# Optimization experiments

Measured on AMD Instinct MI355X. Metric: run time of the kernel, lower is better.

The kernel has to match this reference:

```python
import jax, jax.numpy as jnp
import numpy as np

D = 1024
B = 16
T = 2048
LN_EPS = 1e-5


def setup_inputs() -> dict:
    key = jax.random.key(0)
    k_x, k_in, k_st = jax.random.split(key, 3)
    x = jax.random.normal(k_x, (B, T, D), dtype=jnp.float32)
    # nn.Linear(d, 2d, bias=False): weight [2D, D], y = x @ W.T
    s_in = 1.0 / np.sqrt(D)
    W_in = jax.random.uniform(k_in, (2 * D, D), dtype=jnp.float32, minval=-s_in, maxval=s_in)
    W_state = jax.random.uniform(k_st, (D, D), dtype=jnp.float32, minval=-s_in, maxval=s_in)
    gamma = jnp.ones((D,), dtype=jnp.float32)
    beta = jnp.zeros((D,), dtype=jnp.float32)
    return {"x": x, "W_in": W_in, "W_state": W_state, "gamma": gamma, "beta": beta}


def _glru(x, W_in, W_state, gamma, beta):
    # Batched projections over all timesteps (gates depend only on x).
    proj = jnp.einsum("btd,ed->bte", x, W_in)            # [B, T, 2D]
    gx, vx = jnp.split(proj, 2, axis=-1)                   # each [B, T, D]
    u = jax.nn.sigmoid(gx)                                  # [B, T, D]
    cand = jnp.einsum("btd,ed->bte", vx, W_state)        # [B, T, D]

    # Sequential diagonal linear recurrence: h_t = u_t * h_{t-1} + (1-u_t)*cand_t
    def step(h, uc):
        u_t, c_t = uc
        h = u_t * h + (1.0 - u_t) * c_t
        return h, h

    h0 = jnp.zeros((x.shape[0], x.shape[2]), dtype=x.dtype)
    us = jnp.swapaxes(u, 0, 1)       # [T, B, D]
    cs = jnp.swapaxes(cand, 0, 1)    # [T, B, D]
    _, ys = jax.lax.scan(step, h0, (us, cs))
    y = jnp.swapaxes(ys, 0, 1)       # [B, T, D]

    # LayerNorm over last dim
    mu = jnp.mean(y, axis=-1, keepdims=True)
    var = jnp.mean(jnp.square(y - mu), axis=-1, keepdims=True)
    return (y - mu) * jax.lax.rsqrt(var + LN_EPS) * gamma + beta


def reference(x, W_in, W_state, gamma, beta):
    return _glru(x, W_in, W_state, gamma, beta)
```

## Files before the change

### kernel.cpp

```cpp
#include <hip/hip_runtime.h>

#define D_DIM 1024
#define B_DIM 16
#define T_DIM 2048
#define M_TOT (B_DIM * T_DIM)
#define K_DIM 1024
#define LN_EPS 1e-5f
#define CHUNK 16
#define NCH (T_DIM / CHUNK)

typedef _Float16 half8 __attribute__((ext_vector_type(8)));
typedef _Float16 half4v __attribute__((ext_vector_type(4)));
typedef float f32x4 __attribute__((ext_vector_type(4)));


__global__ __launch_bounds__(256) void prep_all(const float* __restrict__ x,
                                                const float* __restrict__ W_in,
                                                const float* __restrict__ W_state,
                                                _Float16* __restrict__ xh,
                                                _Float16* __restrict__ pk,
                                                _Float16* __restrict__ wvxT,
                                                _Float16* __restrict__ wst) {
    __shared__ _Float16 t[32][33];
    int b = blockIdx.x, tid = threadIdx.x;
    if (b < 2048) {
        int i = b * 256 + tid;
        for (; i < M_TOT * K_DIM / 8; i += 2048 * 256) {
            const float4* p = (const float4*)x + 2 * (size_t)i;
            float4 a = p[0], c = p[1];
            half8 h;
            h[0] = (_Float16)a.x; h[1] = (_Float16)a.y; h[2] = (_Float16)a.z; h[3] = (_Float16)a.w;
            h[4] = (_Float16)c.x; h[5] = (_Float16)c.y; h[6] = (_Float16)c.z; h[7] = (_Float16)c.w;
            ((half8*)xh)[i] = h;
        }
    } else if (b < 2560) {
        int i = (b - 2048) * 256 + tid;
        int ll = i & 63, u = i >> 6;
        int kt = u & 31, nf = u >> 5;
        int n = nf * 16 + (ll & 15);
        int k = kt * 32 + (ll >> 4) * 8;
        const float4* s = (const float4*)&W_in[(size_t)n * 1024 + k];
        float4 a = s[0], c = s[1];
        half8 h;
        h[0] = (_Float16)a.x; h[1] = (_Float16)a.y; h[2] = (_Float16)a.z; h[3] = (_Float16)a.w;
        h[4] = (_Float16)c.x; h[5] = (_Float16)c.y; h[6] = (_Float16)c.z; h[7] = (_Float16)c.w;
        *(half8*)&pk[(size_t)i * 8] = h;
    } else if (b < 3072) {
        int i = (b - 2560) * 256 + tid;
        const float4* p = (const float4*)W_state + 2 * (size_t)i;
        float4 a = p[0], c = p[1];
        half8 h;
        h[0] = (_Float16)a.x; h[1] = (_Float16)a.y; h[2] = (_Float16)a.z; h[3] = (_Float16)a.w;
        h[4] = (_Float16)c.x; h[5] = (_Float16)c.y; h[6] = (_Float16)c.z; h[7] = (_Float16)c.w;
        ((half8*)wst)[i] = h;
    } else {
        int tile = b - 3072;
        int bx = (tile & 31) * 32, by = (tile >> 5) * 32;
        int tx = tid & 31, ty = tid >> 5;
        const float* src = W_in + (size_t)D_DIM * K_DIM;
#pragma unroll
        for (int j = 0; j < 4; ++j)
            t[ty + 8 * j][tx] = (_Float16)src[(size_t)(by + ty + 8 * j) * 1024 + bx + tx];
        __syncthreads();
#pragma unroll
        for (int j = 0; j < 4; ++j)
            wvxT[(size_t)(bx + ty + 8 * j) * 1024 + by + tx] = t[tx][ty + 8 * j];
    }
}

__device__ __forceinline__ void gl_lds16(const _Float16* g, _Float16* l) {
    __builtin_amdgcn_global_load_lds(
        (const __attribute__((address_space(1))) unsigned int*)g,
        (__attribute__((address_space(3))) unsigned int*)l,
        16, 0, 0);
}

__device__ __forceinline__ void stageA32(const _Float16* __restrict__ G,
                                         int row0, int kt,
                                         _Float16* lds0, int wid, int lane) {
    int c = wid * 64 + lane;
    int rl = c >> 2;
    int cc = c & 3;
    int src = cc ^ ((rl >> 1) & 3);
    gl_lds16(G + (size_t)(row0 + rl) * 1024 + kt + src * 8,
             lds0 + (size_t)(wid * 64) * 8);
}

__device__ __forceinline__ half8 frag32(const _Float16* base, int row, int kq) {
    int cc = kq ^ ((row >> 1) & 3);
    return *(const half8*)(base + (size_t)row * 32 + cc * 8);
}

__device__ __forceinline__ half8 bload(const _Float16* __restrict__ pb,
                                       int nf, int kt, int lane) {
    return *(const half8*)(pb + (((size_t)nf * 32 + kt) * 64 + lane) * 8);
}

template <int TA>
__device__ __forceinline__ void gstep(const _Float16* __restrict__ A,
                                      const _Float16* __restrict__ pb,
                                      int m0, int nf0, int t, int nkt,
                                      int wid, int lane, int r, int kq,
                                      _Float16 (&As)[3][64][32],
                                      half8 (&bb)[4],
                                      f32x4 (&acc)[4][4]) {
    half8 ra[4];

    if (t + 1 < nkt) asm volatile("s_waitcnt vmcnt(5)" ::: "memory");
    else             asm volatile("s_waitcnt vmcnt(0)" ::: "memory");
    __builtin_amdgcn_s_barrier();
    __builtin_amdgcn_sched_barrier(0);

#pragma unroll
    for (int mi = 0; mi < 4; mi++) ra[mi] = frag32(&As[TA][0][0], mi * 16 + r, kq);
    if (t + 2 < nkt) stageA32(A, m0, (t + 2) << 5, &As[(TA + 2) % 3][0][0], wid, lane);
    __builtin_amdgcn_s_setprio(1);
#pragma unroll
    for (int mi = 0; mi < 4; mi++)
#pragma unroll
        for (int ni = 0; ni < 4; ni++)
            acc[mi][ni] = __builtin_amdgcn_mfma_f32_16x16x32_f16(ra[mi], bb[ni], acc[mi][ni], 0, 0, 0);
    __builtin_amdgcn_s_setprio(0);
    if (t + 1 < nkt) {
        bb[0] = bload(pb, nf0,      t + 1, lane);
        bb[1] = bload(pb, nf0 + 1,  t + 1, lane);
        bb[2] = bload(pb, nf0 + 64, t + 1, lane);
        bb[3] = bload(pb, nf0 + 65, t + 1, lane);
    }
    __builtin_amdgcn_s_barrier();
}

__global__ __launch_bounds__(256, 3) void gemm256(const _Float16* __restrict__ A,
                                                  const _Float16* __restrict__ pk,
                                                  _Float16* __restrict__ out_u,
                                                  _Float16* __restrict__ out_c,
                                                  float* __restrict__ Ac,
                                                  float* __restrict__ Bc) {
    __shared__ _Float16 As[3][64][32];

    int bid = blockIdx.x;
    int xcd = bid & 7, lin = bid >> 3;
    int mt = xcd * 64 + (lin >> 3);
    int nt = lin & 7;
    int m0 = mt * 64;

    int tid = threadIdx.x, wid = tid >> 6, lane = tid & 63;
    int wc = wid;
    int r = lane & 15, kq = lane >> 4;
    int nf0 = nt * 8 + wc * 2;

    f32x4 acc[4][4];
#pragma unroll
    for (int i = 0; i < 4; i++)
#pragma unroll
        for (int j = 0; j < 4; j++) acc[i][j] = (f32x4)0.f;

    half8 bb[4];
    const int nkt = K_DIM >> 5;

    stageA32(A, m0, 0,  &As[0][0][0], wid, lane);
    stageA32(A, m0, 32, &As[1][0][0], wid, lane);
    bb[0] = bload(pk, nf0,      0, lane);
    bb[1] = bload(pk, nf0 + 1,  0, lane);
    bb[2] = bload(pk, nf0 + 64, 0, lane);
    bb[3] = bload(pk, nf0 + 65, 0, lane);

    for (int t0 = 0; t0 < nkt; t0 += 3) {
        gstep<0>(A, pk, m0, nf0, t0, nkt, wid, lane, r, kq, As, bb, acc);
        if (t0 + 1 < nkt)
            gstep<1>(A, pk, m0, nf0, t0 + 1, nkt, wid, lane, r, kq, As, bb, acc);
        if (t0 + 2 < nkt)
            gstep<2>(A, pk, m0, nf0, t0 + 2, nkt, wid, lane, r, kq, As, bb, acc);
    }

    int rr = kq * 4;
#pragma unroll
    for (int mi = 0; mi < 4; mi++) {
        int mbase = m0 + mi * 16 + rr;
        float Aab[2] = {1.f, 1.f}, Bab[2] = {0.f, 0.f};
#pragma unroll
        for (int ni = 0; ni < 2; ni++) {
            int d = nt * 128 + wc * 32 + ni * 16 + r;
#pragma unroll
            for (int q = 0; q < 4; q++) {
                float u = 1.f / (1.f + __expf(-acc[mi][ni][q]));
                float c = acc[mi][ni + 2][q];
                size_t m = (size_t)(mbase + q);
                out_u[m * D_DIM + d] = (_Float16)u;
                out_c[m * D_DIM + d] = (_Float16)c;
                Bab[ni] = fmaf(u, Bab[ni], (1.f - u) * c);
                Aab[ni] *= u;
            }
        }
#pragma unroll
        for (int ni = 0; ni < 2; ni++) {
            float Aa = Aab[ni], Bb = Bab[ni];
            float oA = __shfl_xor(Aa, 16), oB = __shfl_xor(Bb, 16);
            if (kq & 1) { Bb = fmaf(Aa, oB, Bb); Aa *= oA; }
            else        { Bb = fmaf(oA, Bb, oB); Aa *= oA; }
            oA = __shfl_xor(Aa, 32); oB = __shfl_xor(Bb, 32);
            if (kq & 2) { Bb = fmaf(Aa, oB, Bb); Aa *= oA; }
            else        { Bb = fmaf(oA, Bb, oB); Aa *= oA; }
            if (kq == 0) {
                int d = nt * 128 + wc * 32 + ni * 16 + r;
                int bc = mt * 4 + mi;
                Ac[(size_t)bc * 1024 + d] = Aa;
                Bc[(size_t)bc * 1024 + d] = Bb;
            }
        }
    }
}

__global__ __launch_bounds__(256) void wcomb_splitk(const _Float16* __restrict__ A,
                                                    const _Float16* __restrict__ Bm,
                                                    float* __restrict__ part) {
    __shared__ _Float16 As[128 * 32];
    __shared__ _Float16 Bs[128 * 32];
    int bid = blockIdx.x;
    int mt = bid & 7, nt = (bid >> 3) & 7, sl = bid >> 6;
    int m0 = mt * 128, n0 = nt * 128, kbeg = sl * 256;
    int tid = threadIdx.x, wid = tid >> 6, lane = tid & 63;
    int wr = wid >> 1, wc = wid & 1;

    f32x4 acc[4][4];
#pragma unroll
    for (int i = 0; i < 4; i++)
#pragma unroll
        for (int j = 0; j < 4; j++) acc[i][j] = (f32x4)0.f;

    int r = lane & 15, kq = lane >> 4;

    for (int kt = kbeg; kt < kbeg + 256; kt += 32) {
        __syncthreads();
#pragma unroll
        for (int j = 0; j < 2; ++j) {
            int f = j * 256 + tid;
            int row = f >> 2, kc = f & 3;
            gl_lds16(A + (size_t)(m0 + row) * 1024 + kt + kc * 8, As + (size_t)(j * 256 + wid * 64) * 8);
            gl_lds16(Bm + (size_t)(n0 + row) * 1024 + kt + kc * 8, Bs + (size_t)(j * 256 + wid * 64) * 8);
        }
        __syncthreads();
        half8 af[4], bf[4];
#pragma unroll
        for (int mi = 0; mi < 4; mi++) af[mi] = *(const half8*)&As[(wr * 64 + mi * 16 + r) * 32 + kq * 8];
#pragma unroll
        for (int ni = 0; ni < 4; ni++) bf[ni] = *(const half8*)&Bs[(wc * 64 + ni * 16 + r) * 32 + kq * 8];
#pragma unroll
        for (int mi = 0; mi < 4; mi++)
#pragma unroll
            for (int ni = 0; ni < 4; ni++)
                acc[mi][ni] = __builtin_amdgcn_mfma_f32_16x16x32_f16(af[mi], bf[ni], acc[mi][ni], 0, 0, 0);
    }

    int rr = kq * 4;
    float* pbp = part + (size_t)sl * 1048576;
#pragma unroll
    for (int mi = 0; mi < 4; mi++) {
        int mbase = m0 + wr * 64 + mi * 16 + rr;
#pragma unroll
        for (int ni = 0; ni < 4; ni++) {
            int n = n0 + wc * 64 + ni * 16 + r;
#pragma unroll
            for (int q = 0; q < 4; q++)
                pbp[(size_t)(mbase + q) * 1024 + n] = acc[mi][ni][q];
        }
    }
}

__global__ __launch_bounds__(256) void wcomb_combine_pack(const float* __restrict__ part,
                                                          _Float16* __restrict__ pk) {
    int i = blockIdx.x * 256 + threadIdx.x;
    int ll = i & 63, u = i >> 6;
    int kt = u & 31, nf = u >> 5;
    int e = nf * 16 + (ll & 15);
    int k = kt * 32 + (ll >> 4) * 8;
    size_t o = (size_t)e * 1024 + k;
    float s[8];
#pragma unroll
    for (int j = 0; j < 8; ++j) s[j] = 0.f;
#pragma unroll
    for (int sl = 0; sl < 4; ++sl) {
        const float4* p = (const float4*)&part[(size_t)sl * 1048576 + o];
        float4 a = p[0], c = p[1];
        s[0] += a.x; s[1] += a.y; s[2] += a.z; s[3] += a.w;
        s[4] += c.x; s[5] += c.y; s[6] += c.z; s[7] += c.w;
    }
    half8 h;
#pragma unroll
    for (int j = 0; j < 8; ++j) h[j] = (_Float16)s[j];
    *(half8*)&pk[1048576 + (size_t)i * 8] = h;
}

__global__ __launch_bounds__(256) void scan_pass2(const float* __restrict__ Ac,
                                                  const float* __restrict__ Bc,
                                                  float* __restrict__ h0w) {
    int idx = blockIdx.x * 256 + threadIdx.x;
    int b = idx >> 10, d = idx & (D_DIM - 1);
    float h = 0.f;
#pragma unroll 8
    for (int ch = 0; ch < NCH; ++ch) {
        size_t k = ((size_t)(b * NCH + ch) << 10) + d;
        float a = Ac[k];
        float bv = Bc[k];
        h0w[k] = h;
        h = fmaf(a, h, bv);
    }
}

__global__ __launch_bounds__(64) void scan_ln(const _Float16* __restrict__ u,
                                              const _Float16* __restrict__ cd,
                                              const float* __restrict__ h0,
                                              const float* __restrict__ gamma,
                                              const float* __restrict__ beta,
                                              float* __restrict__ outp) {
    int bc = blockIdx.x;
    int b = bc >> 7, ch = bc & (NCH - 1);
    int lane = threadIdx.x;
    int d0 = lane * 16;
    size_t base = ((size_t)b * T_DIM + (size_t)ch * CHUNK) * D_DIM + d0;

    float g[16], be[16], h[16];
#pragma unroll
    for (int j = 0; j < 16; j += 4) {
        *(float4*)&g[j]  = *(const float4*)&gamma[d0 + j];
        *(float4*)&be[j] = *(const float4*)&beta[d0 + j];
    }
    size_t o = (size_t)bc * D_DIM + d0;
#pragma unroll
    for (int j = 0; j < 16; j += 4) *(float4*)&h[j] = *(const float4*)&h0[o + j];

    half8 ua = *(const half8*)&u[base];
    half8 ub = *(const half8*)&u[base + 8];
    half8 ca = *(const half8*)&cd[base];
    half8 cb = *(const half8*)&cd[base + 8];

#pragma unroll
    for (int t = 0; t < CHUNK; ++t) {
        half8 nua, nub, nca, ncb;
        if (t + 1 < CHUNK) {
            size_t nrow = base + (size_t)(t + 1) * D_DIM;
            nua = *(const half8*)&u[nrow];
            nub = *(const half8*)&u[nrow + 8];
            nca = *(const half8*)&cd[nrow];
            ncb = *(const half8*)&cd[nrow + 8];
        }
        size_t row = base + (size_t)t * D_DIM;
        float s = 0.f, q = 0.f;
#pragma unroll
        for (int j = 0; j < 8; ++j) {
            float ut = (float)ua[j], ct = (float)ca[j];
            h[j] = fmaf(ut, h[j] - ct, ct);
            s += h[j]; q += h[j] * h[j];
        }
#pragma unroll
        for (int j = 0; j < 8; ++j) {
            float ut = (float)ub[j], ct = (float)cb[j];
            h[8 + j] = fmaf(ut, h[8 + j] - ct, ct);
            s += h[8 + j]; q += h[8 + j] * h[8 + j];
        }
#pragma unroll
        for (int off = 32; off > 0; off >>= 1) {
            s += __shfl_xor(s, off);
            q += __shfl_xor(q, off);
        }
        float mu = s * (1.f / D_DIM);
        float var = q * (1.f / D_DIM) - mu * mu;
        float rs = rsqrtf(var + LN_EPS);
        float o16[16];
#pragma unroll
        for (int j = 0; j < 16; ++j) o16[j] = (h[j] - mu) * rs * g[j] + be[j];
#pragma unroll
        for (int j = 0; j < 16; j += 4) *(float4*)&outp[row + j] = *(float4*)&o16[j];
        ua = nua; ub = nub; ca = nca; cb = ncb;
    }
}

extern "C" void kernel_launch(void* const* d_in, const int* in_sizes, int n_in,
                              void* d_out, int out_size, void* d_ws, size_t ws_size,
                              hipStream_t stream) {
    const float* x       = (const float*)d_in[0];
    const float* W_in    = (const float*)d_in[1];
    const float* W_state = (const float*)d_in[2];
    const float* gamma   = (const float*)d_in[3];
    const float* beta    = (const float*)d_in[4];
    float* out = (float*)d_out;

    char* w = (char*)d_ws;
    size_t off = 0;
    auto carve = [&](size_t bytes) {
        void* p = w + off;
        off += (bytes + 255) & ~(size_t)255;
        return p;
    };
    _Float16* xh   = (_Float16*)carve((size_t)M_TOT * K_DIM * 2);
    _Float16* pk   = (_Float16*)carve((size_t)2 * D_DIM * K_DIM * 2);
    _Float16* uarr = (_Float16*)carve((size_t)M_TOT * D_DIM * 2);
    _Float16* cand = (_Float16*)carve((size_t)M_TOT * D_DIM * 2);
    char* scratch  = (char*)carve((size_t)16 * 1024 * 1024);
    _Float16* wvxT = (_Float16*)scratch;
    _Float16* wst  = (_Float16*)(scratch + 2 * 1024 * 1024);
    float* Ac = (float*)scratch;
    float* Bc = (float*)(scratch + 8 * 1024 * 1024);
    float* wpart = (float*)cand;
    float* h0w = (float*)xh;

    prep_all<<<4096, 256, 0, stream>>>(x, W_in, W_state, xh, pk, wvxT, wst);

    wcomb_splitk<<<256, 256, 0, stream>>>(wst, wvxT, wpart);
    wcomb_combine_pack<<<512, 256, 0, stream>>>(wpart, pk);

    gemm256<<<4096, 256, 0, stream>>>(xh, pk, uarr, cand, Ac, Bc);

    scan_pass2<<<(B_DIM * D_DIM) / 256, 256, 0, stream>>>(Ac, Bc, h0w);
    scan_ln<<<B_DIM * NCH, 64, 0, stream>>>(uarr, cand, h0w, gamma, beta, out);
}
```

Before: 296.9 us.

## Double GEMM K-tile to 64 with 8-way XOR-swizzled LDS staging

```diff
diff --git a/kernel.cpp b/kernel.cpp
--- a/kernel.cpp
+++ b/kernel.cpp
@@ -75,20 +75,25 @@
         16, 0, 0);
 }
 
-__device__ __forceinline__ void stageA32(const _Float16* __restrict__ G,
+
+__device__ __forceinline__ void stageA64(const _Float16* __restrict__ G,
                                          int row0, int kt,
                                          _Float16* lds0, int wid, int lane) {
-    int c = wid * 64 + lane;
-    int rl = c >> 2;
-    int cc = c & 3;
-    int src = cc ^ ((rl >> 1) & 3);
-    gl_lds16(G + (size_t)(row0 + rl) * 1024 + kt + src * 8,
-             lds0 + (size_t)(wid * 64) * 8);
-}
-
-__device__ __forceinline__ half8 frag32(const _Float16* base, int row, int kq) {
-    int cc = kq ^ ((row >> 1) & 3);
-    return *(const half8*)(base + (size_t)row * 32 + cc * 8);
+#pragma unroll
+    for (int call = 0; call < 2; ++call) {
+        int c0 = call * 256 + wid * 64;
+        int c  = c0 + lane;
+        int rl = c >> 3;
+        int cc = c & 7;
+        int src = cc ^ (rl & 7);
+        gl_lds16(G + (size_t)(row0 + rl) * 1024 + kt + src * 8,
+                 lds0 + (size_t)c0 * 8);
+    }
+}
+
+__device__ __forceinline__ half8 frag64(const _Float16* base, int row, int ksub, int kq) {
+    int pc = ((ksub << 2) | kq) ^ (row & 7);
+    return *(const half8*)(base + (size_t)row * 64 + pc * 8);
 }
 
 __device__ __forceinline__ half8 bload(const _Float16* __restrict__ pb,
@@ -101,31 +106,46 @@
                                       const _Float16* __restrict__ pb,
                                       int m0, int nf0, int t, int nkt,
                                       int wid, int lane, int r, int kq,
-                                      _Float16 (&As)[3][64][32],
-                                      half8 (&bb)[4],
+                                      _Float16 (&As)[3][64][64],
+                                      half8 (&bb)[8],
                                       f32x4 (&acc)[4][4]) {
-    half8 ra[4];
-
-    if (t + 1 < nkt) asm volatile("s_waitcnt vmcnt(5)" ::: "memory");
-    else             asm volatile("s_waitcnt vmcnt(0)" ::: "memory");
+    half8 ra0[4], ra1[4];
+
+    if (t + 1 < nkt) asm volatile("s_waitcnt vmcnt(10)" ::: "memory");
+    else             asm volatile("s_waitcnt vmcnt(8)"  ::: "memory");
     __builtin_amdgcn_s_barrier();
     __builtin_amdgcn_sched_barrier(0);
 
 #pragma unroll
-    for (int mi = 0; mi < 4; mi++) ra[mi] = frag32(&As[TA][0][0], mi * 16 + r, kq);
-    if (t + 2 < nkt) stageA32(A, m0, (t + 2) << 5, &As[(TA + 2) % 3][0][0], wid, lane);
+    for (int mi = 0; mi < 4; mi++) ra0[mi] = frag64(&As[TA][0][0], mi * 16 + r, 0, kq);
+    if (t + 2 < nkt) stageA64(A, m0, (t + 2) << 6, &As[(TA + 2) % 3][0][0], wid, lane);
     __builtin_amdgcn_s_setprio(1);
 #pragma unroll
     for (int mi = 0; mi < 4; mi++)
 #pragma unroll
         for (int ni = 0; ni < 4; ni++)
-            acc[mi][ni] = __builtin_amdgcn_mfma_f32_16x16x32_f16(ra[mi], bb[ni], acc[mi][ni], 0, 0, 0);
+            acc[mi][ni] = __builtin_amdgcn_mfma_f32_16x16x32_f16(ra0[mi], bb[ni], acc[mi][ni], 0, 0, 0);
+    __builtin_amdgcn_s_setprio(0);
+
+#pragma unroll
+    for (int mi = 0; mi < 4; mi++) ra1[mi] = frag64(&As[TA][0][0], mi * 16 + r, 1, kq);
+    __builtin_amdgcn_s_setprio(1);
+#pragma unroll
+    for (int mi = 0; mi < 4; mi++)
+#pragma unroll
+        for (int ni = 0; ni < 4; ni++)
+            acc[mi][ni] = __builtin_amdgcn_mfma_f32_16x16x32_f16(ra1[mi], bb[4 + ni], acc[mi][ni], 0, 0, 0);
     __builtin_amdgcn_s_setprio(0);
     if (t + 1 < nkt) {
-        bb[0] = bload(pb, nf0,      t + 1, lane);
-        bb[1] = bload(pb, nf0 + 1,  t + 1, lane);
-        bb[2] = bload(pb, nf0 + 64, t + 1, lane);
-        bb[3] = bload(pb, nf0 + 65, t + 1, lane);
+        int k0 = (t + 1) << 1;
+        bb[0] = bload(pb, nf0,      k0,     lane);
+        bb[1] = bload(pb, nf0 + 1,  k0,     lane);
+        bb[2] = bload(pb, nf0 + 64, k0,     lane);
+        bb[3] = bload(pb, nf0 + 65, k0,     lane);
+        bb[4] = bload(pb, nf0,      k0 + 1, lane);
+        bb[5] = bload(pb, nf0 + 1,  k0 + 1, lane);
+        bb[6] = bload(pb, nf0 + 64, k0 + 1, lane);
+        bb[7] = bload(pb, nf0 + 65, k0 + 1, lane);
     }
     __builtin_amdgcn_s_barrier();
 }
@@ -136,7 +156,7 @@
                                                   _Float16* __restrict__ out_c,
                                                   float* __restrict__ Ac,
                                                   float* __restrict__ Bc) {
-    __shared__ _Float16 As[3][64][32];
+    __shared__ _Float16 As[3][64][64];
 
     int bid = blockIdx.x;
     int xcd = bid & 7, lin = bid >> 3;
@@ -155,15 +175,19 @@
 #pragma unroll
         for (int j = 0; j < 4; j++) acc[i][j] = (f32x4)0.f;
 
-    half8 bb[4];
-    const int nkt = K_DIM >> 5;
-
-    stageA32(A, m0, 0,  &As[0][0][0], wid, lane);
-    stageA32(A, m0, 32, &As[1][0][0], wid, lane);
+    half8 bb[8];
+    const int nkt = K_DIM >> 6;
+
+    stageA64(A, m0, 0,  &As[0][0][0], wid, lane);
+    stageA64(A, m0, 64, &As[1][0][0], wid, lane);
     bb[0] = bload(pk, nf0,      0, lane);
     bb[1] = bload(pk, nf0 + 1,  0, lane);
     bb[2] = bload(pk, nf0 + 64, 0, lane);
     bb[3] = bload(pk, nf0 + 65, 0, lane);
+    bb[4] = bload(pk, nf0,      1, lane);
+    bb[5] = bload(pk, nf0 + 1,  1, lane);
+    bb[6] = bload(pk, nf0 + 64, 1, lane);
+    bb[7] = bload(pk, nf0 + 65, 1, lane);
 
     for (int t0 = 0; t0 < nkt; t0 += 3) {
         gstep<0>(A, pk, m0, nf0, t0, nkt, wid, lane, r, kq, As, bb, acc);
```

Result: no change. 291.4 us (-1.9%).
